# Optimization experiments

Hardware: AMD Instinct MI355X
Metric: run time of the kernel (lower is better)

## Reference

```python
import jax, jax.numpy as jnp
import numpy as np

NEG_BIG = -9e15
ALPHA = 0.2  # leaky relu slope


def setup_inputs() -> dict:
    key = jax.random.key(0)
    k1, k2, k3, k4 = jax.random.split(key, 4)
    B, N, F_in, F_out = 4, 4096, 256, 128
    h = jax.random.normal(k1, (B, N, F_in), dtype=jnp.float32)
    adj = jax.random.randint(k2, (B, N, N), 0, 2, dtype=jnp.int32)
    W = jax.random.normal(k3, (F_in, F_out), dtype=jnp.float32) * (1.0 / np.sqrt(F_in))
    a = jax.random.normal(k4, (2 * F_out,), dtype=jnp.float32) * (1.0 / np.sqrt(2 * F_out))
    return {"h": h, "adj": adj, "W": W, "a": a}


def reference(h, adj, W, a):
    F_out = W.shape[1]
    Wh = jnp.einsum("bnf,fo->bno", h, W)                    # [B,N,F_out]
    # split-a trick: a^T [Wh_i ; Wh_j] = a1.Wh_i + a2.Wh_j (same math as concat)
    f1 = Wh @ a[:F_out]                                       # [B,N] source (row) term
    f2 = Wh @ a[F_out:]                                       # [B,N] target (col) term
    e = jax.nn.leaky_relu(f1[:, :, None] + f2[:, None, :], negative_slope=ALPHA)
    e = jnp.where(adj > 0, e, NEG_BIG)
    attention = jax.nn.softmax(e, axis=-1)                   # [B,N,N]
    h_prime = jnp.einsum("bnm,bmo->bno", attention, Wh)      # [B,N,F_out]
    return jax.nn.elu(h_prime)
```

## Files before the change

### kernel.cpp

```cpp
#include <hip/hip_runtime.h>
#include <hip/hip_bf16.h>

#define B_ 4
#define N_ 4096
#define FIN 256
#define FOUT 128

typedef unsigned short u16;
typedef short bf16x8 __attribute__((ext_vector_type(8)));
typedef float f32x4 __attribute__((ext_vector_type(4)));
typedef int i32x4 __attribute__((ext_vector_type(4)));

__device__ __forceinline__ u16 f2bf(float x) {
  union { float f; unsigned int u; } v;
  v.f = x;
  unsigned int r = v.u + 0x7fffu + ((v.u >> 16) & 1u);
  return (u16)(r >> 16);
}

__device__ __forceinline__ unsigned int pk2(float a, float b) {
  union { __hip_bfloat162 h2; unsigned int u; } v;
  v.h2 = __float22bfloat162_rn(make_float2(a, b));
  return v.u;
}

__global__ __launch_bounds__(256) void wh_kernel(
    const float* __restrict__ h, const float* __restrict__ W,
    const float* __restrict__ a, u16* __restrict__ whT,
    float* __restrict__ f1, float* __restrict__ f2) {
  __shared__ float hs[16 * FIN];
  const int tid = threadIdx.x;
  const int b = blockIdx.x >> 8;
  const int n0 = (blockIdx.x & 255) << 4;

  {
    const float4* src = (const float4*)(h + ((size_t)(b * N_ + n0)) * FIN);
    float4* dst = (float4*)hs;
#pragma unroll
    for (int i = 0; i < 4; ++i) dst[tid + i * 256] = src[tid + i * 256];
  }
  __syncthreads();

  const int o0 = (tid & 31) * 4;
  const int r0 = tid >> 5;
  float acc0[4] = {0.f, 0.f, 0.f, 0.f};
  float acc1[4] = {0.f, 0.f, 0.f, 0.f};
  const float* hr0 = hs + r0 * FIN;
  const float* hr1 = hs + (r0 + 8) * FIN;
#pragma unroll 4
  for (int k = 0; k < FIN; ++k) {
    const float4 w = *(const float4*)(W + k * FOUT + o0);
    const float h0 = hr0[k];
    const float h1 = hr1[k];
    acc0[0] = fmaf(h0, w.x, acc0[0]); acc0[1] = fmaf(h0, w.y, acc0[1]);
    acc0[2] = fmaf(h0, w.z, acc0[2]); acc0[3] = fmaf(h0, w.w, acc0[3]);
    acc1[0] = fmaf(h1, w.x, acc1[0]); acc1[1] = fmaf(h1, w.y, acc1[1]);
    acc1[2] = fmaf(h1, w.z, acc1[2]); acc1[3] = fmaf(h1, w.w, acc1[3]);
  }

  float s10 = 0.f, s11 = 0.f, s20 = 0.f, s21 = 0.f;
#pragma unroll
  for (int j = 0; j < 4; ++j) {
    const float a1v = a[o0 + j];
    const float a2v = a[FOUT + o0 + j];
    s10 = fmaf(acc0[j], a1v, s10); s20 = fmaf(acc0[j], a2v, s20);
    s11 = fmaf(acc1[j], a1v, s11); s21 = fmaf(acc1[j], a2v, s21);
  }
#pragma unroll
  for (int off = 16; off >= 1; off >>= 1) {
    s10 += __shfl_xor(s10, off); s11 += __shfl_xor(s11, off);
    s20 += __shfl_xor(s20, off); s21 += __shfl_xor(s21, off);
  }
  if ((tid & 31) == 0) {
    const int base = b * N_ + n0;
    f1[base + r0] = s10; f1[base + r0 + 8] = s11;
    f2[base + r0] = s20; f2[base + r0 + 8] = s21;
  }

  __syncthreads();
  u16* ts = (u16*)hs;
#pragma unroll
  for (int j = 0; j < 4; ++j) {
    ts[(o0 + j) * 16 + r0]     = f2bf(acc0[j]);
    ts[(o0 + j) * 16 + r0 + 8] = f2bf(acc1[j]);
  }
  __syncthreads();
  const int o  = tid >> 1;
  const int hh = tid & 1;
  const uint4 vals = *(const uint4*)(ts + o * 16 + hh * 8);
  u16* dst = whT + ((size_t)((b * 512 + (n0 >> 3) + hh) * 128 + o)) * 8;
  *(uint4*)dst = vals;
}

__device__ __forceinline__ float pv_(int m, float t) {
  const float e = fmaxf(t, 0.2f * t);
  const float ex = __expf(e);
  return m > 0 ? ex : 0.f;
}

__global__ __launch_bounds__(256) void gat_kernel(
    const int* __restrict__ adj, const u16* __restrict__ whT,
    const float* __restrict__ f1, const float* __restrict__ f2,
    float* __restrict__ out) {
  __shared__ float red[9360];
  const int tid = threadIdx.x;
  const int wave = tid >> 6;
  const int lane = tid & 63;
  const int b = blockIdx.x >> 8;
  const int i0 = (blockIdx.x & 255) << 4;
  const int row = lane & 15;
  const int kg = lane >> 4;
  const int j0 = wave << 10;

  const float f1r = f1[b * N_ + i0 + row];
  const i32x4* ap = (const i32x4*)(adj + ((size_t)(b * N_ + i0 + row)) * N_ + j0 + kg * 8);
  const float4* fp = (const float4*)(f2 + b * N_ + j0 + kg * 8);
  const u16* wp = whT + ((size_t)((b * 512 + (j0 >> 3) + kg) * 128 + row)) * 8;

  f32x4 acc[9];
#pragma unroll
  for (int i = 0; i < 9; ++i) acc[i] = (f32x4){0.f, 0.f, 0.f, 0.f};
  bf16x8 ones;
#pragma unroll
  for (int i = 0; i < 8; ++i) ones[i] = (short)0x3F80;

  auto compute = [&](i32x4 a0, i32x4 a1, float4 fa, float4 fb) {
    bf16x8 bf0 = *(const bf16x8*)(wp);
    bf16x8 bf1 = *(const bf16x8*)(wp + 128);
    bf16x8 bf2 = *(const bf16x8*)(wp + 256);
    bf16x8 bf3 = *(const bf16x8*)(wp + 384);
    bf16x8 bf4 = *(const bf16x8*)(wp + 512);
    bf16x8 bf5 = *(const bf16x8*)(wp + 640);
    bf16x8 bf6 = *(const bf16x8*)(wp + 768);
    bf16x8 bf7 = *(const bf16x8*)(wp + 896);
    const float p0 = pv_(a0[0], f1r + fa.x);
    const float p1 = pv_(a0[1], f1r + fa.y);
    const float p2 = pv_(a0[2], f1r + fa.z);
    const float p3 = pv_(a0[3], f1r + fa.w);
    const float p4 = pv_(a1[0], f1r + fb.x);
    const float p5 = pv_(a1[1], f1r + fb.y);
    const float p6 = pv_(a1[2], f1r + fb.z);
    const float p7 = pv_(a1[3], f1r + fb.w);
    union { bf16x8 v; unsigned int u[4]; } pf;
    pf.u[0] = pk2(p0, p1); pf.u[1] = pk2(p2, p3);
    pf.u[2] = pk2(p4, p5); pf.u[3] = pk2(p6, p7);
    __builtin_amdgcn_s_setprio(1);
    acc[0] = __builtin_amdgcn_mfma_f32_16x16x32_bf16(pf.v, bf0, acc[0], 0, 0, 0);
    acc[1] = __builtin_amdgcn_mfma_f32_16x16x32_bf16(pf.v, bf1, acc[1], 0, 0, 0);
    acc[2] = __builtin_amdgcn_mfma_f32_16x16x32_bf16(pf.v, bf2, acc[2], 0, 0, 0);
    acc[3] = __builtin_amdgcn_mfma_f32_16x16x32_bf16(pf.v, bf3, acc[3], 0, 0, 0);
    acc[4] = __builtin_amdgcn_mfma_f32_16x16x32_bf16(pf.v, bf4, acc[4], 0, 0, 0);
    acc[5] = __builtin_amdgcn_mfma_f32_16x16x32_bf16(pf.v, bf5, acc[5], 0, 0, 0);
    acc[6] = __builtin_amdgcn_mfma_f32_16x16x32_bf16(pf.v, bf6, acc[6], 0, 0, 0);
    acc[7] = __builtin_amdgcn_mfma_f32_16x16x32_bf16(pf.v, bf7, acc[7], 0, 0, 0);
    acc[8] = __builtin_amdgcn_mfma_f32_16x16x32_bf16(pf.v, ones, acc[8], 0, 0, 0);
    __builtin_amdgcn_s_setprio(0);
    wp += 4096;
  };

  i32x4 a0_0 = __builtin_nontemporal_load(ap);
  i32x4 a1_0 = __builtin_nontemporal_load(ap + 1);
  float4 fa_0 = fp[0], fb_0 = fp[1];
  ap += 8; fp += 8;
  i32x4 a0_1 = __builtin_nontemporal_load(ap);
  i32x4 a1_1 = __builtin_nontemporal_load(ap + 1);
  float4 fa_1 = fp[0], fb_1 = fp[1];

  for (int s = 0; s < 15; ++s) {
    ap += 8; fp += 8;
    i32x4 na0 = __builtin_nontemporal_load(ap);
    i32x4 na1 = __builtin_nontemporal_load(ap + 1);
    float4 nfa = fp[0], nfb = fp[1];
    compute(a0_0, a1_0, fa_0, fb_0);
    a0_0 = na0; a1_0 = na1; fa_0 = nfa; fb_0 = nfb;

    ap += 8; fp += 8;
    na0 = __builtin_nontemporal_load(ap);
    na1 = __builtin_nontemporal_load(ap + 1);
    nfa = fp[0]; nfb = fp[1];
    compute(a0_1, a1_1, fa_1, fb_1);
    a0_1 = na0; a1_1 = na1; fa_1 = nfa; fb_1 = nfb;
  }
  compute(a0_0, a1_0, fa_0, fb_0);
  compute(a0_1, a1_1, fa_1, fb_1);

#pragma unroll
  for (int fi = 0; fi < 9; ++fi)
    *(f32x4*)&red[(wave * 9 + fi) * 260 + lane * 4] = acc[fi];
  __syncthreads();

  const int i = tid >> 4;
  const int oo = (tid & 15) * 8;
  const int lnb = (i >> 2) << 4;
  const int rg = i & 3;
  float lt = 0.f;
#pragma unroll
  for (int w = 0; w < 4; ++w) lt += red[(w * 9 + 8) * 260 + lnb * 4 + rg];
  const float inv = 1.f / lt;
  float res[8];
#pragma unroll
  for (int jo = 0; jo < 8; ++jo) {
    const int o = oo + jo;
    const int fi = o >> 4;
    const int lidx = lnb + (o & 15);
    float sacc = 0.f;
#pragma unroll
    for (int w = 0; w < 4; ++w)
      sacc += red[(w * 9 + fi) * 260 + lidx * 4 + rg];
    const float x = sacc * inv;
    res[jo] = x > 0.f ? x : expm1f(x);
  }
  float4* op = (float4*)(out + ((size_t)(b * N_ + i0 + i)) * FOUT + oo);
  op[0] = make_float4(res[0], res[1], res[2], res[3]);
  op[1] = make_float4(res[4], res[5], res[6], res[7]);
}

extern "C" void kernel_launch(void* const* d_in, const int* in_sizes, int n_in,
                              void* d_out, int out_size, void* d_ws, size_t ws_size,
                              hipStream_t stream) {
  const float* h = (const float*)d_in[0];
  const int* adj = (const int*)d_in[1];
  const float* W = (const float*)d_in[2];
  const float* a = (const float*)d_in[3];
  float* out = (float*)d_out;

  u16* whT = (u16*)d_ws;
  float* f1 = (float*)((char*)d_ws + (size_t)B_ * FOUT * N_ * sizeof(u16));
  float* f2 = f1 + B_ * N_;

  wh_kernel<<<dim3(B_ * (N_ / 16)), dim3(256), 0, stream>>>(h, W, a, whT, f1, f2);
  gat_kernel<<<dim3(B_ * (N_ / 16)), dim3(256), 0, stream>>>(adj, whT, f1, f2, out);
}
```

Before: 452.6 us.

## Pre-pack adjacency into bitmasks in a separate kernel before attention

Adds a pack kernel that reads the int32 adjacency matrix once and writes one 32-bit mask word per 32 columns. The attention kernel then loads a single u32 per step and extracts its 8 bits by shifting, instead of issuing two 16-byte nontemporal loads per lane. This is meant to take the large adjacency stream out of the MFMA/exp inner loop and shrink its register and latency footprint. The full adjacency read still happens every call, and there is now an extra launch plus an 8 MB workspace round trip.

```diff
diff --git a/kernel.cpp b/kernel.cpp
--- a/kernel.cpp
+++ b/kernel.cpp
@@ -7,6 +7,7 @@
 #define FOUT 128
 
 typedef unsigned short u16;
+typedef unsigned int u32;
 typedef short bf16x8 __attribute__((ext_vector_type(8)));
 typedef float f32x4 __attribute__((ext_vector_type(4)));
 typedef int i32x4 __attribute__((ext_vector_type(4)));
@@ -92,14 +93,30 @@
   *(uint4*)dst = vals;
 }
 
-__device__ __forceinline__ float pv_(int m, float t) {
+__global__ __launch_bounds__(256) void pack_kernel(
+    const int* __restrict__ adj, u32* __restrict__ pw) {
+  const size_t gid = (size_t)blockIdx.x * 256 + threadIdx.x;
+  const i32x4* src = (const i32x4*)(adj + gid * 32);
+  u32 m = 0;
+#pragma unroll
+  for (int c = 0; c < 8; ++c) {
+    const i32x4 v = __builtin_nontemporal_load(src + c);
+    m |= (v[0] > 0 ? 1u : 0u) << (c * 4 + 0);
+    m |= (v[1] > 0 ? 1u : 0u) << (c * 4 + 1);
+    m |= (v[2] > 0 ? 1u : 0u) << (c * 4 + 2);
+    m |= (v[3] > 0 ? 1u : 0u) << (c * 4 + 3);
+  }
+  pw[gid] = m;
+}
+
+__device__ __forceinline__ float pv2(u32 bit, float t) {
   const float e = fmaxf(t, 0.2f * t);
   const float ex = __expf(e);
-  return m > 0 ? ex : 0.f;
+  return bit ? ex : 0.f;
 }
 
 __global__ __launch_bounds__(256) void gat_kernel(
-    const int* __restrict__ adj, const u16* __restrict__ whT,
+    const u32* __restrict__ pw, const u16* __restrict__ whT,
     const float* __restrict__ f1, const float* __restrict__ f2,
     float* __restrict__ out) {
   __shared__ float red[9360];
@@ -111,10 +128,11 @@
   const int row = lane & 15;
   const int kg = lane >> 4;
   const int j0 = wave << 10;
+  const int ksh = kg << 3;
 
   const float f1r = f1[b * N_ + i0 + row];
-  const i32x4* ap = (const i32x4*)(adj + ((size_t)(b * N_ + i0 + row)) * N_ + j0 + kg * 8);
-  const float4* fp = (const float4*)(f2 + b * N_ + j0 + kg * 8);
+  const u32* mp = pw + ((size_t)(b * N_ + i0 + row)) * 128 + wave * 32;
+  const float4* fp = (const float4*)(f2 + b * N_ + j0 + (kg << 3));
   const u16* wp = whT + ((size_t)((b * 512 + (j0 >> 3) + kg) * 128 + row)) * 8;
 
   f32x4 acc[9];
@@ -124,7 +142,7 @@
 #pragma unroll
   for (int i = 0; i < 8; ++i) ones[i] = (short)0x3F80;
 
-  auto compute = [&](i32x4 a0, i32x4 a1, float4 fa, float4 fb) {
+  auto compute = [&](u32 mw, float4 fa, float4 fb) {
     bf16x8 bf0 = *(const bf16x8*)(wp);
     bf16x8 bf1 = *(const bf16x8*)(wp + 128);
     bf16x8 bf2 = *(const bf16x8*)(wp + 256);
@@ -133,14 +151,15 @@
     bf16x8 bf5 = *(const bf16x8*)(wp + 640);
     bf16x8 bf6 = *(const bf16x8*)(wp + 768);
     bf16x8 bf7 = *(const bf16x8*)(wp + 896);
-    const float p0 = pv_(a0[0], f1r + fa.x);
-    const float p1 = pv_(a0[1], f1r + fa.y);
-    const float p2 = pv_(a0[2], f1r + fa.z);
-    const float p3 = pv_(a0[3], f1r + fa.w);
-    const float p4 = pv_(a1[0], f1r + fb.x);
-    const float p5 = pv_(a1[1], f1r + fb.y);
-    const float p6 = pv_(a1[2], f1r + fb.z);
-    const float p7 = pv_(a1[3], f1r + fb.w);
+    const u32 mb = mw >> ksh;
+    const float p0 = pv2(mb & 1u,        f1r + fa.x);
+    const float p1 = pv2((mb >> 1) & 1u, f1r + fa.y);
+    const float p2 = pv2((mb >> 2) & 1u, f1r + fa.z);
+    const float p3 = pv2((mb >> 3) & 1u, f1r + fa.w);
+    const float p4 = pv2((mb >> 4) & 1u, f1r + fb.x);
+    const float p5 = pv2((mb >> 5) & 1u, f1r + fb.y);
+    const float p6 = pv2((mb >> 6) & 1u, f1r + fb.z);
+    const float p7 = pv2((mb >> 7) & 1u, f1r + fb.w);
     union { bf16x8 v; unsigned int u[4]; } pf;
     pf.u[0] = pk2(p0, p1); pf.u[1] = pk2(p2, p3);
     pf.u[2] = pk2(p4, p5); pf.u[3] = pk2(p6, p7);
@@ -158,31 +177,24 @@
     wp += 4096;
   };
 
-  i32x4 a0_0 = __builtin_nontemporal_load(ap);
-  i32x4 a1_0 = __builtin_nontemporal_load(ap + 1);
+  u32 m_0 = mp[0];
   float4 fa_0 = fp[0], fb_0 = fp[1];
-  ap += 8; fp += 8;
-  i32x4 a0_1 = __builtin_nontemporal_load(ap);
-  i32x4 a1_1 = __builtin_nontemporal_load(ap + 1);
-  float4 fa_1 = fp[0], fb_1 = fp[1];
+  u32 m_1 = mp[1];
+  float4 fa_1 = fp[8], fb_1 = fp[9];
 
   for (int s = 0; s < 15; ++s) {
-    ap += 8; fp += 8;
-    i32x4 na0 = __builtin_nontemporal_load(ap);
-    i32x4 na1 = __builtin_nontemporal_load(ap + 1);
-    float4 nfa = fp[0], nfb = fp[1];
-    compute(a0_0, a1_0, fa_0, fb_0);
-    a0_0 = na0; a1_0 = na1; fa_0 = nfa; fb_0 = nfb;
-
-    ap += 8; fp += 8;
-    na0 = __builtin_nontemporal_load(ap);
-    na1 = __builtin_nontemporal_load(ap + 1);
-    nfa = fp[0]; nfb = fp[1];
-    compute(a0_1, a1_1, fa_1, fb_1);
-    a0_1 = na0; a1_1 = na1; fa_1 = nfa; fb_1 = nfb;
-  }
-  compute(a0_0, a1_0, fa_0, fb_0);
-  compute(a0_1, a1_1, fa_1, fb_1);
+    u32 nm = mp[2 * s + 2];
+    float4 nfa = fp[16 * s + 16], nfb = fp[16 * s + 17];
+    compute(m_0, fa_0, fb_0);
+    m_0 = nm; fa_0 = nfa; fb_0 = nfb;
+
+    nm = mp[2 * s + 3];
+    nfa = fp[16 * s + 24]; nfb = fp[16 * s + 25];
+    compute(m_1, fa_1, fb_1);
+    m_1 = nm; fa_1 = nfa; fb_1 = nfb;
+  }
+  compute(m_0, fa_0, fb_0);
+  compute(m_1, fa_1, fb_1);
 
 #pragma unroll
   for (int fi = 0; fi < 9; ++fi)
@@ -224,10 +236,14 @@
   const float* a = (const float*)d_in[3];
   float* out = (float*)d_out;
 
-  u16* whT = (u16*)d_ws;
-  float* f1 = (float*)((char*)d_ws + (size_t)B_ * FOUT * N_ * sizeof(u16));
+  char* wsb = (char*)d_ws;
+  u16* whT = (u16*)wsb;
+  float* f1 = (float*)(wsb + (size_t)B_ * FOUT * N_ * sizeof(u16));
   float* f2 = f1 + B_ * N_;
-
+  u32* pw = (u32*)(wsb + (size_t)B_ * FOUT * N_ * sizeof(u16)
+                   + 2 * (size_t)B_ * N_ * sizeof(float));
+
+  pack_kernel<<<dim3(B_ * N_ * 128 / 256), dim3(256), 0, stream>>>(adj, pw);
   wh_kernel<<<dim3(B_ * (N_ / 16)), dim3(256), 0, stream>>>(h, W, a, whT, f1, f2);
-  gat_kernel<<<dim3(B_ * (N_ / 16)), dim3(256), 0, stream>>>(adj, whT, f1, f2, out);
-}
+  gat_kernel<<<dim3(B_ * (N_ / 16)), dim3(256), 0, stream>>>(pw, whT, f1, f2, out);
+}
```

Result: slower. 498.4 us (+10.1%).
